# Kernel optimization log

Measured on AMD Instinct MI355X. Metric: run time of the kernel, lower is better.

Reference implementation:

```python
import jax, jax.numpy as jnp
import numpy as np


def setup_inputs() -> dict:
    key = jax.random.key(0)
    k1, k2, k3, k4 = jax.random.split(key, 4)
    B, D, H, W, M = 16, 512, 96, 96, 128
    x = jax.random.normal(k1, (B, D, H, W), dtype=jnp.float32)
    evolved_feat = jax.random.normal(k2, (B, M, D), dtype=jnp.float32)
    # 1x1 conv over 2*D channels -> 1 channel: weight [2D], bias [1]
    conv_w = jax.random.normal(k3, (2 * D,), dtype=jnp.float32) * (1.0 / np.sqrt(2 * D))
    conv_b = jax.random.normal(k4, (1,), dtype=jnp.float32) * 0.01
    return {"x": x, "evolved_feat": evolved_feat, "conv_w": conv_w, "conv_b": conv_b}


def reference(x, evolved_feat, conv_w, conv_b):
    # x: [B, D, H, W], evolved_feat: [B, M, D]
    B, D, H, W = x.shape
    M = evolved_feat.shape[1]
    # conv1x1 over concat([x_pixel, evolve_node]) == split dot products, broadcast-added
    wA, wB = conv_w[:D], conv_w[D:]
    x_flat = x.reshape(B, D, H * W).transpose(0, 2, 1)       # [B, HW, D]
    s_pix = x_flat @ wA                                      # [B, HW]
    s_node = evolved_feat @ wB                               # [B, M]
    scores = s_pix[:, :, None] + s_node[:, None, :] + conv_b[0]  # [B, HW, M]
    # original softmax is over dim=0 of the [HW, M] per-batch matrix -> axis=1 here
    mapping = jax.nn.softmax(scores, axis=1)                 # [B, HW, M]
    out = jax.nn.relu(jnp.einsum('bpm,bmd->bpd', mapping, evolved_feat))  # [B, HW, D]
    out = out.reshape(B, H, W, D).transpose(0, 3, 1, 2)      # [B, D, H, W]
    return out
```

## Files before the change

### kernel.cpp

```cpp
#include <hip/hip_runtime.h>
#include <math.h>

#define Bn 16
#define Dn 512
#define Hn 96
#define Wn 96
#define Pn (Hn * Wn)
#define Mn 128

#define DZ 4
#define DCH (Dn / DZ)
#define PC 9
#define NCHUNK 36
#define DG 4
#define NJ 9

typedef float vfloat4 __attribute__((ext_vector_type(4)));

__global__ void k_spix4(const float* __restrict__ x, const float* __restrict__ conv_w,
                        float* __restrict__ partial) {
    __shared__ float wA[DCH];
    const int b  = blockIdx.x;
    const int pc = blockIdx.y;
    const int dz = blockIdx.z;
    const int t  = threadIdx.x;
    if (t < DCH) wA[t] = conv_w[dz * DCH + t];
    __syncthreads();

    const int p = pc * 1024 + t * 4;
    const float* xb = x + ((size_t)(b * Dn + dz * DCH)) * Pn + p;
    vfloat4 acc = {0.f, 0.f, 0.f, 0.f};
#pragma unroll 8
    for (int d = 0; d < DCH; ++d) {
        vfloat4 v = __builtin_nontemporal_load((const vfloat4*)(xb + (size_t)d * Pn));
        const float wv = wA[d];
        acc.x = fmaf(v.x, wv, acc.x);
        acc.y = fmaf(v.y, wv, acc.y);
        acc.z = fmaf(v.z, wv, acc.z);
        acc.w = fmaf(v.w, wv, acc.w);
    }
    *(vfloat4*)(partial + ((size_t)(b * DZ + dz)) * Pn + p) = acc;
}

__global__ void k_finish(const float* __restrict__ partial, const float* __restrict__ ef,
                         float* __restrict__ w, float* __restrict__ pexp,
                         float* __restrict__ E) {
    __shared__ float red[256];
    const int b = blockIdx.x;
    const int c = blockIdx.y;
    const int t = threadIdx.x;
    const int p = c * 256 + t;
    const size_t base = (size_t)b * DZ * Pn + p;
    const float s = partial[base] + partial[base + Pn] +
                    partial[base + 2 * Pn] + partial[base + 3 * Pn];
    const float e = __expf(s);
    w[b * Pn + p] = e;
    red[t] = e;
    __syncthreads();
    for (int o = 128; o > 0; o >>= 1) {
        if (t < o) red[t] += red[t + o];
        __syncthreads();
    }
    if (t == 0) pexp[b * NCHUNK + c] = red[0];

    if (c < 2) {
        const int d = c * 256 + t;
        const float* q = ef + (size_t)b * Mn * Dn + d;
        float sE = 0.f;
#pragma unroll 16
        for (int m = 0; m < Mn; ++m) sE += q[(size_t)m * Dn];
        E[b * Dn + d] = sE;
    }
}

__global__ void k_out(const float* __restrict__ w, const float* __restrict__ E,
                      const float* __restrict__ pexp, float* __restrict__ out) {
    const int b  = blockIdx.x;
    const int dg = blockIdx.y * DG;
    const int t  = threadIdx.x;

    float denom = 0.f;
#pragma unroll
    for (int j = 0; j < NCHUNK; ++j) denom += pexp[b * NCHUNK + j];
    const float inv = 1.f / denom;

    const vfloat4* w4 = (const vfloat4*)(w + b * Pn);
    vfloat4 wv[NJ];
#pragma unroll
    for (int j = 0; j < NJ; ++j) wv[j] = w4[t + 256 * j];

    vfloat4* o4 = (vfloat4*)(out + ((size_t)(b * Dn + dg)) * Pn);
#pragma unroll
    for (int r = 0; r < DG; ++r) {
        const float evr = fmaxf(E[b * Dn + dg + r], 0.f) * inv;
        vfloat4* orow = o4 + (size_t)r * (Pn / 4);
#pragma unroll
        for (int j = 0; j < NJ; ++j) {
            orow[t + 256 * j] = wv[j] * evr;
        }
    }
}

extern "C" void kernel_launch(void* const* d_in, const int* in_sizes, int n_in,
                              void* d_out, int out_size, void* d_ws, size_t ws_size,
                              hipStream_t stream) {
    const float* x      = (const float*)d_in[0];
    const float* ef     = (const float*)d_in[1];
    const float* conv_w = (const float*)d_in[2];

    float* out = (float*)d_out;

    float* w       = (float*)d_ws;
    float* E       = w + Bn * Pn;
    float* partial = E + Bn * Dn;
    float* pexp    = partial + (size_t)Bn * DZ * Pn;
    (void)in_sizes; (void)n_in; (void)out_size; (void)ws_size;

    k_spix4<<<dim3(Bn, PC, DZ), dim3(256), 0, stream>>>(x, conv_w, partial);

    k_finish<<<dim3(Bn, NCHUNK), dim3(256), 0, stream>>>(partial, ef, w, pexp, E);

    k_out<<<dim3(Bn, Dn / DG), dim3(256), 0, stream>>>(w, E, pexp, out);
}
```

Baseline: 109.4 us.

## Fuse pixel-score reduction and softmax-exp into one 1024-thread kernel

Merges the split-D pixel dot-product kernel and the finish kernel into one launch. Each 1024-thread block now covers all four D sub-ranges of a pixel chunk and combines their partial sums in shared memory before applying exp and the block reduction. The E column sums move into one extra block per batch. This removes the global partial buffer round trip and one kernel launch. In exchange, the grid drops to 160 large blocks, which may leave many CUs idle during the memory-bound read of x.

```diff
diff --git a/kernel.cpp b/kernel.cpp
--- a/kernel.cpp
+++ b/kernel.cpp
@@ -8,68 +8,69 @@
 #define Pn (Hn * Wn)
 #define Mn 128
 
-#define DZ 4
-#define DCH (Dn / DZ)
-#define PC 9
-#define NCHUNK 36
+#define NCHUNK 9
+#define SUBG 4
+#define DCH (Dn / SUBG)
 #define DG 4
 #define NJ 9
 
 typedef float vfloat4 __attribute__((ext_vector_type(4)));
 
-__global__ void k_spix4(const float* __restrict__ x, const float* __restrict__ conv_w,
-                        float* __restrict__ partial) {
-    __shared__ float wA[DCH];
+__global__ void k_spix_fused(const float* __restrict__ x, const float* __restrict__ conv_w,
+                             const float* __restrict__ ef,
+                             float* __restrict__ w, float* __restrict__ pexp,
+                             float* __restrict__ E) {
     const int b  = blockIdx.x;
     const int pc = blockIdx.y;
-    const int dz = blockIdx.z;
     const int t  = threadIdx.x;
-    if (t < DCH) wA[t] = conv_w[dz * DCH + t];
-    __syncthreads();
 
-    const int p = pc * 1024 + t * 4;
-    const float* xb = x + ((size_t)(b * Dn + dz * DCH)) * Pn + p;
-    vfloat4 acc = {0.f, 0.f, 0.f, 0.f};
+    if (pc < NCHUNK) {
+        __shared__ float   wA_s[Dn];
+        __shared__ vfloat4 acc_s[SUBG - 1][256];
+        __shared__ float   red[256];
+        const int sg = t >> 8;
+        const int tt = t & 255;
+        if (t < Dn) wA_s[t] = conv_w[t];
+        __syncthreads();
+
+        const int p = pc * 1024 + tt * 4;
+        const float* xb = x + ((size_t)(b * Dn + sg * DCH)) * Pn + p;
+        vfloat4 acc = {0.f, 0.f, 0.f, 0.f};
 #pragma unroll 8
-    for (int d = 0; d < DCH; ++d) {
-        vfloat4 v = __builtin_nontemporal_load((const vfloat4*)(xb + (size_t)d * Pn));
-        const float wv = wA[d];
-        acc.x = fmaf(v.x, wv, acc.x);
-        acc.y = fmaf(v.y, wv, acc.y);
-        acc.z = fmaf(v.z, wv, acc.z);
-        acc.w = fmaf(v.w, wv, acc.w);
-    }
-    *(vfloat4*)(partial + ((size_t)(b * DZ + dz)) * Pn + p) = acc;
-}
-
-__global__ void k_finish(const float* __restrict__ partial, const float* __restrict__ ef,
-                         float* __restrict__ w, float* __restrict__ pexp,
-                         float* __restrict__ E) {
-    __shared__ float red[256];
-    const int b = blockIdx.x;
-    const int c = blockIdx.y;
-    const int t = threadIdx.x;
-    const int p = c * 256 + t;
-    const size_t base = (size_t)b * DZ * Pn + p;
-    const float s = partial[base] + partial[base + Pn] +
-                    partial[base + 2 * Pn] + partial[base + 3 * Pn];
-    const float e = __expf(s);
-    w[b * Pn + p] = e;
-    red[t] = e;
-    __syncthreads();
-    for (int o = 128; o > 0; o >>= 1) {
-        if (t < o) red[t] += red[t + o];
+        for (int d = 0; d < DCH; ++d) {
+            vfloat4 v = __builtin_nontemporal_load((const vfloat4*)(xb + (size_t)d * Pn));
+            const float wv = wA_s[sg * DCH + d];
+            acc.x = fmaf(v.x, wv, acc.x);
+            acc.y = fmaf(v.y, wv, acc.y);
+            acc.z = fmaf(v.z, wv, acc.z);
+            acc.w = fmaf(v.w, wv, acc.w);
+        }
+        if (sg > 0) acc_s[sg - 1][tt] = acc;
         __syncthreads();
-    }
-    if (t == 0) pexp[b * NCHUNK + c] = red[0];
-
-    if (c < 2) {
-        const int d = c * 256 + t;
-        const float* q = ef + (size_t)b * Mn * Dn + d;
-        float sE = 0.f;
+        if (sg == 0) {
+            vfloat4 s4 = acc + acc_s[0][tt] + acc_s[1][tt] + acc_s[2][tt];
+            vfloat4 e4;
+            e4.x = __expf(s4.x);
+            e4.y = __expf(s4.y);
+            e4.z = __expf(s4.z);
+            e4.w = __expf(s4.w);
+            *(vfloat4*)(w + b * Pn + p) = e4;
+            red[tt] = (e4.x + e4.y) + (e4.z + e4.w);
+        }
+        __syncthreads();
+        for (int o = 128; o > 0; o >>= 1) {
+            if (t < o) red[t] += red[t + o];
+            __syncthreads();
+        }
+        if (t == 0) pexp[b * NCHUNK + pc] = red[0];
+    } else {
+        if (t < Dn) {
+            const float* q = ef + (size_t)b * Mn * Dn + t;
+            float sE = 0.f;
 #pragma unroll 16
-        for (int m = 0; m < Mn; ++m) sE += q[(size_t)m * Dn];
-        E[b * Dn + d] = sE;
+            for (int m = 0; m < Mn; ++m) sE += q[(size_t)m * Dn];
+            E[b * Dn + t] = sE;
+        }
     }
 }
 
@@ -110,15 +111,13 @@
 
     float* out = (float*)d_out;
 
-    float* w       = (float*)d_ws;
-    float* E       = w + Bn * Pn;
-    float* partial = E + Bn * Dn;
-    float* pexp    = partial + (size_t)Bn * DZ * Pn;
+    float* w    = (float*)d_ws;
+    float* E    = w + Bn * Pn;
+    float* pexp = E + Bn * Dn;
     (void)in_sizes; (void)n_in; (void)out_size; (void)ws_size;
 
-    k_spix4<<<dim3(Bn, PC, DZ), dim3(256), 0, stream>>>(x, conv_w, partial);
-
-    k_finish<<<dim3(Bn, NCHUNK), dim3(256), 0, stream>>>(partial, ef, w, pexp, E);
+    k_spix_fused<<<dim3(Bn, NCHUNK + 1), dim3(1024), 0, stream>>>(
+        x, conv_w, ef, w, pexp, E);
 
     k_out<<<dim3(Bn, Dn / DG), dim3(256), 0, stream>>>(w, E, pexp, out);
 }
```

Result: faster. 100.2 us (-8.4%).
